# Kernel optimization log

Measured on AMD Instinct MI355X. Metric: run time of the kernel, lower is better.

## Reference

```python
import jax, jax.numpy as jnp
import numpy as np
from jax import lax

B, T, C = 4, 1024, 1024
NH, HD = 16, 64
SCALE = 1.0 / np.sqrt(HD)
LN_EPS = 1e-5


def _layernorm(x, g, b):
    mu = jnp.mean(x, axis=-1, keepdims=True)
    var = jnp.var(x, axis=-1, keepdims=True)
    return (x - mu) * lax.rsqrt(var + LN_EPS) * g + b


def _compress(seg, w, g, b):
    # seg: [B, nH, L, hd]; depthwise Conv1d(k=2, s=2, p=1, groups=hd, no bias) + LayerNorm(hd)
    Bs, nH, L, hd = seg.shape
    xc = seg.reshape(Bs * nH, L, hd).transpose(0, 2, 1)  # [B*nH, hd, L]
    y = lax.conv_general_dilated(xc, w, window_strides=(2,), padding=[(1, 1)],
                                 dimension_numbers=('NCH', 'OIH', 'NCH'),
                                 feature_group_count=hd)  # [B*nH, hd, L//2+1]
    y = y.transpose(0, 2, 1)
    y = _layernorm(y, g, b)
    return y.reshape(Bs, nH, -1, hd)


def setup_inputs() -> dict:
    key = jax.random.key(0)
    ks = jax.random.split(key, 16)
    d = {
        'x': jax.random.normal(ks[0], (B, T, C), jnp.float32),
        'mem_k1': jax.random.normal(ks[1], (B, NH, 129, HD), jnp.float32),
        'mem_v1': jax.random.normal(ks[2], (B, NH, 129, HD), jnp.float32),
        'mem_k2': jax.random.normal(ks[3], (B, NH, 257, HD), jnp.float32),
        'mem_v2': jax.random.normal(ks[4], (B, NH, 257, HD), jnp.float32),
        'mem_k3': jax.random.normal(ks[5], (B, NH, 513, HD), jnp.float32),
        'mem_v3': jax.random.normal(ks[6], (B, NH, 513, HD), jnp.float32),
        'c_attn_w': jax.random.normal(ks[7], (3 * C, C), jnp.float32) * 0.02,
        'c_attn_b': jnp.zeros((3 * C,), jnp.float32),
        'c_proj_w': jax.random.normal(ks[8], (C, C), jnp.float32) * 0.02,
        'c_proj_b': jnp.zeros((C,), jnp.float32),
        'compress_k_w': jax.random.normal(ks[9], (HD, 1, 2), jnp.float32) * 0.5,
        'ln_k_g': jnp.ones((HD,), jnp.float32),
        'ln_k_b': jnp.zeros((HD,), jnp.float32),
        'compress_v_w': jax.random.normal(ks[10], (HD, 1, 2), jnp.float32) * 0.5,
        'ln_v_g': jnp.ones((HD,), jnp.float32),
        'ln_v_b': jnp.zeros((HD,), jnp.float32),
    }
    return d


def reference(x, mem_k1, mem_v1, mem_k2, mem_v2, mem_k3, mem_v3,
              c_attn_w, c_attn_b, c_proj_w, c_proj_b,
              compress_k_w, ln_k_g, ln_k_b, compress_v_w, ln_v_g, ln_v_b):
    # qkv projection
    qkv = x @ c_attn_w.T + c_attn_b  # [B, T, 3C]
    q, k_new, v_new = jnp.split(qkv, 3, axis=2)
    q = q.reshape(B, T, NH, HD).transpose(0, 2, 1, 3)       # [B, nH, T, hd]
    k_new = k_new.reshape(B, T, NH, HD).transpose(0, 2, 1, 3)
    v_new = v_new.reshape(B, T, NH, HD).transpose(0, 2, 1, 3)

    # compress the most recent cached segment (513 -> 257)
    k3c = _compress(mem_k3, compress_k_w, ln_k_g, ln_k_b)
    v3c = _compress(mem_v3, compress_v_w, ln_v_g, ln_v_b)

    all_k = jnp.concatenate([mem_k1, mem_k2, k3c, k_new], axis=2)  # [B, nH, T_mem, hd]
    all_v = jnp.concatenate([mem_v1, mem_v2, v3c, v_new], axis=2)
    T_mem = all_k.shape[2]

    att = jnp.einsum('bhqd,bhkd->bhqk', q, all_k) * SCALE  # [B, nH, T, T_mem]
    # causal mask taken from tril(block_size)[:T, :T_mem]: row i attends cols j <= i
    mask = jnp.arange(T)[:, None] >= jnp.arange(T_mem)[None, :]
    att = jnp.where(mask, att, -jnp.inf)
    att = jax.nn.softmax(att, axis=-1)
    y = jnp.einsum('bhqk,bhkd->bhqd', att, all_v)  # [B, nH, T, hd]
    y = y.transpose(0, 2, 1, 3).reshape(B, T, C)
    y = y @ c_proj_w.T + c_proj_b
    return y
```

## Files before the change

kernel.cpp:

```cpp
#include <hip/hip_runtime.h>


using u16    = unsigned short;
using bf16x8 = __attribute__((ext_vector_type(8))) __bf16;
using f32x4  = __attribute__((ext_vector_type(4))) float;
using u16x8  = __attribute__((ext_vector_type(8))) unsigned short;
using u16x4  = __attribute__((ext_vector_type(4))) unsigned short;

__device__ __forceinline__ u16 f2bf(float f) {
    union { float f; unsigned u; } v; v.f = f;
    unsigned r = v.u + 0x7FFFu + ((v.u >> 16) & 1u);
    return (u16)(r >> 16);
}

__device__ __forceinline__ void gload16(const void* src, const void* lds_base) {
    __builtin_amdgcn_global_load_lds(
        (const __attribute__((address_space(1))) void*)src,
        (__attribute__((address_space(3))) void*)lds_base, 16, 0, 0);
}

__global__ void cvt_f32_bf16(const float* __restrict__ src, u16* __restrict__ dst, int n4) {
    int i = blockIdx.x * blockDim.x + threadIdx.x;
    if (i >= n4) return;
    float4 f = reinterpret_cast<const float4*>(src)[i];
    u16x4 o; o[0] = f2bf(f.x); o[1] = f2bf(f.y); o[2] = f2bf(f.z); o[3] = f2bf(f.w);
    reinterpret_cast<u16x4*>(dst)[i] = o;
}

__global__ __launch_bounds__(64) void copy_mem_rows(const float* __restrict__ src,
                                                    u16* __restrict__ dst, int L, int ro) {
    int bh = blockIdx.y, t = blockIdx.x, d = threadIdx.x;
    float v = src[((size_t)bh * L + t) * 64 + d];
    dst[((size_t)bh * 1024 + ro + t) * 64 + d] = f2bf(v);
}

__global__ __launch_bounds__(64) void compress_ln(const float* __restrict__ src,
                                                  const float* __restrict__ w,
                                                  const float* __restrict__ g,
                                                  const float* __restrict__ bta,
                                                  u16* __restrict__ dst, int ro) {
    int bh = blockIdx.y, t = blockIdx.x, d = threadIdx.x;
    const float* seg = src + (size_t)bh * 513 * 64;
    float x0 = (t > 0) ? seg[(size_t)(2 * t - 1) * 64 + d] : 0.f;
    float x1 = seg[(size_t)(2 * t) * 64 + d];
    float y = w[2 * d] * x0 + w[2 * d + 1] * x1;
    float s = y;
    #pragma unroll
    for (int o = 32; o; o >>= 1) s += __shfl_xor(s, o);
    float mu = s * (1.f / 64.f);
    float dv = y - mu;
    float s2 = dv * dv;
    #pragma unroll
    for (int o = 32; o; o >>= 1) s2 += __shfl_xor(s2, o);
    float var = s2 * (1.f / 64.f);
    float out = dv * rsqrtf(var + 1e-5f) * g[d] + bta[d];
    dst[((size_t)bh * 1024 + ro + t) * 64 + d] = f2bf(out);
}

__global__ __launch_bounds__(256) void transpose_v(const u16* __restrict__ src,
                                                   u16* __restrict__ dst) {
    __shared__ u16 tile[64][66];
    const int bh = blockIdx.y, t0 = blockIdx.x * 64;
    const int tid = threadIdx.x;
    #pragma unroll
    for (int i = 0; i < 2; ++i) {
        int p = tid + i * 256;
        int tr = p >> 3, dc = (p & 7) * 8;
        *(u16x8*)&tile[tr][dc] = *(const u16x8*)&src[((size_t)bh * 1024 + t0 + tr) * 64 + dc];
    }
    __syncthreads();
    #pragma unroll
    for (int i = 0; i < 2; ++i) {
        int p = tid + i * 256;
        int d = p >> 3, tc = (p & 7) * 8;
        u16x8 v;
        #pragma unroll
        for (int e = 0; e < 8; ++e) v[e] = tile[tc + e][d];
        *(u16x8*)&dst[((size_t)bh * 64 + d) * 1024 + t0 + tc] = v;
    }
}

__global__ __launch_bounds__(256) void gemm128(const u16* __restrict__ A,
                                               const u16* __restrict__ Bw,
                                               const float* __restrict__ bias,
                                               int K, int N, int mode,
                                               float* __restrict__ outF,
                                               u16* __restrict__ q_buf,
                                               u16* __restrict__ all_k,
                                               u16* __restrict__ all_v) {
    __shared__ __align__(16) u16 Al[3][128 * 32];
    __shared__ __align__(16) u16 Bl[3][128 * 32];
    const int tid = threadIdx.x;
    const int wv = tid >> 6, lane = tid & 63;
    const int lg = lane >> 4, lr = lane & 15;
    const int wr = (wv >> 1) * 64, wc = (wv & 1) * 64;
    const int id = blockIdx.x + blockIdx.y * gridDim.x;
    const int gx = gridDim.x;
    const int pm = gx >> 2;
    const int xcd = id & 7, lid = id >> 3;
    const int mg = xcd >> 1, ng = xcd & 1;
    const int lm = lid % pm, ln = lid / pm;
    const int m0 = (mg * pm + lm) * 128;
    const int n0 = (ng * (gridDim.y >> 1) + ln) * 128;
    f32x4 acc[4][4] = {};
    const int sr0 = tid >> 2,         sc0 = ((tid & 3) << 4) ^ (((sr0 >> 1) & 3) << 4);
    const int sr1 = (tid + 256) >> 2, sc1 = ((tid & 3) << 4) ^ (((sr1 >> 1) & 3) << 4);
    const int dA0 = wv * 1024;
    const int dA1 = 4096 + wv * 1024;
    const int nk = K >> 5;

    auto stage = [&](int j) {
        const size_t ko = (size_t)j << 5;
        char* Ad = (char*)&Al[j % 3][0];
        char* Bd = (char*)&Bl[j % 3][0];
        gload16((const char*)A  + (((size_t)(m0 + sr0) * K + ko) << 1) + sc0, Ad + dA0);
        gload16((const char*)A  + (((size_t)(m0 + sr1) * K + ko) << 1) + sc1, Ad + dA1);
        gload16((const char*)Bw + (((size_t)(n0 + sr0) * K + ko) << 1) + sc0, Bd + dA0);
        gload16((const char*)Bw + (((size_t)(n0 + sr1) * K + ko) << 1) + sc1, Bd + dA1);
    };
    stage(0);
    stage(1);
    asm volatile("s_waitcnt vmcnt(4)" ::: "memory");
    __builtin_amdgcn_s_barrier();
    __builtin_amdgcn_sched_barrier(0);

    for (int kt = 0; kt < nk; ++kt) {
        if (kt + 2 < nk) stage(kt + 2);
        const char* At = (const char*)&Al[kt % 3][0];
        const char* Bt = (const char*)&Bl[kt % 3][0];
        bf16x8 af[4], bq[4];
        #pragma unroll
        for (int mi = 0; mi < 4; ++mi) {
            int row = wr + mi * 16 + lr;
            af[mi] = *(const bf16x8*)(At + row * 64 + ((lg << 4) ^ (((row >> 1) & 3) << 4)));
        }
        #pragma unroll
        for (int ni = 0; ni < 4; ++ni) {
            int row = wc + ni * 16 + lr;
            bq[ni] = *(const bf16x8*)(Bt + row * 64 + ((lg << 4) ^ (((row >> 1) & 3) << 4)));
        }
        __builtin_amdgcn_s_setprio(1);
        #pragma unroll
        for (int mi = 0; mi < 4; ++mi)
            #pragma unroll
            for (int ni = 0; ni < 4; ++ni)
                acc[mi][ni] = __builtin_amdgcn_mfma_f32_16x16x32_bf16(af[mi], bq[ni], acc[mi][ni], 0, 0, 0);
        __builtin_amdgcn_s_setprio(0);
        if (kt + 1 < nk) {
            if (kt + 2 < nk) {
                asm volatile("s_waitcnt vmcnt(4)" ::: "memory");
            } else {
                asm volatile("s_waitcnt vmcnt(0)" ::: "memory");
            }
            __builtin_amdgcn_s_barrier();
            __builtin_amdgcn_sched_barrier(0);
        }
    }
    #pragma unroll
    for (int mi = 0; mi < 4; ++mi)
        #pragma unroll
        for (int ni = 0; ni < 4; ++ni)
            #pragma unroll
            for (int r = 0; r < 4; ++r) {
                int mm = m0 + wr + mi * 16 + lg * 4 + r;
                int nn = n0 + wc + ni * 16 + lr;
                float v = acc[mi][ni][r] + bias[nn];
                if (mode == 0) {
                    outF[(size_t)mm * N + nn] = v;
                } else {
                    int which = nn >> 10, c = nn & 1023, h = c >> 6, d = c & 63;
                    int b = mm >> 10, t = mm & 1023;
                    int bh = b * 16 + h;
                    if (which == 0) {
                        q_buf[((size_t)bh * 1024 + t) * 64 + d] = f2bf(v * 0.125f);
                    } else if (t < 381) {
                        u16* dst = (which == 1) ? all_k : all_v;
                        dst[((size_t)bh * 1024 + 643 + t) * 64 + d] = f2bf(v);
                    }
                }
            }
}

__global__ __launch_bounds__(256) void attn_kernel(const u16* __restrict__ Q,
                                                   const u16* __restrict__ Kc,
                                                   const u16* __restrict__ VT,
                                                   u16* __restrict__ Y) {
    __shared__ __align__(16) u16 Kl[2][4096];
    __shared__ __align__(16) u16 Vl[2][4096];
    __shared__ __align__(16) u16 P_w[4][16 * 64];
    const int tid = threadIdx.x;
    const int lane = tid & 63;
    const int w = tid >> 6;
    const int lg = lane >> 4, lr = lane & 15;
    const int bh = blockIdx.x;
    const int pair = blockIdx.y;
    const u16* Kb = Kc + (size_t)bh * 65536;
    const u16* Vb = VT + (size_t)bh * 65536;
    char* Pbase = (char*)&P_w[w][0];
    const int xorq = (lr & 7) << 4;

    const int r0 = tid >> 3,         c0 = ((tid & 7) * 16) ^ ((r0 & 7) << 4);
    const int r1 = (tid + 256) >> 3, c1 = ((tid & 7) * 16) ^ ((r1 & 7) << 4);
    const int dst0 = w * 1024;

    for (int phase = 0; phase < 2; ++phase) {
        const int qt = phase ? (15 - pair) : pair;
        const int q0 = qt * 64;
        const u16* Qb = Q + ((size_t)bh * 1024 + q0 + w * 16) * 64;
        bf16x8 qf0 = *(const bf16x8*)&Qb[lr * 64 + lg * 8];
        bf16x8 qf1 = *(const bf16x8*)&Qb[lr * 64 + 32 + lg * 8];
        f32x4 o[4] = {};
        float m = -1e30f, lsum = 0.f;
        const int i_q = q0 + w * 16 + lr;

        {
            const char* Ks = (const char*)Kb;
            gload16(Ks + ((size_t)r0 << 7) + c0, (char*)&Kl[0][0] + dst0);
            gload16(Ks + ((size_t)r1 << 7) + c1, (char*)&Kl[0][0] + 4096 + dst0);
            gload16((const char*)Vb + ((size_t)r0 << 11) + c0, (char*)&Vl[0][0] + dst0);
            gload16((const char*)Vb + ((size_t)r1 << 11) + c1, (char*)&Vl[0][0] + 4096 + dst0);
        }
        __syncthreads();
        int cur = 0;

        for (int kt = 0; kt <= qt; ++kt) {
            if (kt < qt) {
                const int k0n = (kt + 1) * 64;
                const char* Ks = (const char*)Kb + ((size_t)k0n << 7);
                const char* Vs = (const char*)Vb + ((size_t)k0n << 1);
                char* Kd = (char*)&Kl[cur ^ 1][0];
                char* Vd = (char*)&Vl[cur ^ 1][0];
                gload16(Ks + ((size_t)r0 << 7) + c0, Kd + dst0);
                gload16(Ks + ((size_t)r1 << 7) + c1, Kd + 4096 + dst0);
                gload16(Vs + ((size_t)r0 << 11) + c0, Vd + dst0);
                gload16(Vs + ((size_t)r1 << 11) + c1, Vd + 4096 + dst0);
            }
            const char* Kt = (const char*)&Kl[cur][0];
            const char* Vt = (const char*)&Vl[cur][0];
            f32x4 st[4] = {};
            __builtin_amdgcn_s_setprio(1);
            #pragma unroll
            for (int hh = 0; hh < 4; ++hh) {
                const char* Kr = Kt + (size_t)(hh * 16 + lr) * 128;
                bf16x8 kf0 = *(const bf16x8*)(Kr + ((lg * 16) ^ xorq));
                bf16x8 kf1 = *(const bf16x8*)(Kr + ((64 + lg * 16) ^ xorq));
                st[hh] = __builtin_amdgcn_mfma_f32_16x16x32_bf16(kf0, qf0, st[hh], 0, 0, 0);
                st[hh] = __builtin_amdgcn_mfma_f32_16x16x32_bf16(kf1, qf1, st[hh], 0, 0, 0);
            }
            __builtin_amdgcn_s_setprio(0);
            const int k0 = kt * 64;
            float sv[16];
            float tmax = -1e30f;
            if (kt == qt) {
                #pragma unroll
                for (int hh = 0; hh < 4; ++hh)
                    #pragma unroll
                    for (int r = 0; r < 4; ++r) {
                        int j = k0 + hh * 16 + lg * 4 + r;
                        float s = (j <= i_q) ? st[hh][r] : -1e30f;
                        sv[hh * 4 + r] = s;
                        tmax = fmaxf(tmax, s);
                    }
            } else {
                #pragma unroll
                for (int hh = 0; hh < 4; ++hh)
                    #pragma unroll
                    for (int r = 0; r < 4; ++r) {
                        float s = st[hh][r];
                        sv[hh * 4 + r] = s;
                        tmax = fmaxf(tmax, s);
                    }
            }
            tmax = fmaxf(tmax, __shfl_xor(tmax, 16));
            tmax = fmaxf(tmax, __shfl_xor(tmax, 32));
            if (!__all(tmax - m <= 8.f)) {
                float mnew = fmaxf(m, tmax);
                float alpha = __expf(m - mnew);
                #pragma unroll
                for (int c = 0; c < 4; ++c) {
                    o[c][0] *= alpha; o[c][1] *= alpha; o[c][2] *= alpha; o[c][3] *= alpha;
                }
                lsum *= alpha;
                m = mnew;
            }
            float psum = 0.f;
            #pragma unroll
            for (int hh = 0; hh < 4; ++hh) {
                u16x4 pk;
                #pragma unroll
                for (int r = 0; r < 4; ++r) {
                    float p = __expf(sv[hh * 4 + r] - m);
                    psum += p;
                    pk[r] = f2bf(p);
                }
                *(u16x4*)(Pbase + lr * 128 + ((hh * 32 + lg * 8) ^ xorq)) = pk;
            }
            psum += __shfl_xor(psum, 16);
            psum += __shfl_xor(psum, 32);
            lsum += psum;
            asm volatile("s_waitcnt lgkmcnt(0)" ::: "memory");
            __builtin_amdgcn_sched_barrier(0);
            #pragma unroll
            for (int ks = 0; ks < 2; ++ks) {
                bf16x8 pf = *(const bf16x8*)(Pbase + lr * 128 + ((ks * 64 + lg * 16) ^ xorq));
                __builtin_amdgcn_s_setprio(1);
                #pragma unroll
                for (int c = 0; c < 4; ++c) {
                    const char* Vr = Vt + (size_t)(c * 16 + lr) * 128;
                    bf16x8 vf = *(const bf16x8*)(Vr + ((ks * 64 + lg * 16) ^ xorq));
                    o[c] = __builtin_amdgcn_mfma_f32_16x16x32_bf16(vf, pf, o[c], 0, 0, 0);
                }
                __builtin_amdgcn_s_setprio(0);
            }
            __syncthreads();
            cur ^= 1;
        }
        float inv = 1.0f / lsum;
        #pragma unroll
        for (int c = 0; c < 4; ++c) {
            u16x4 ov;
            #pragma unroll
            for (int r = 0; r < 4; ++r) ov[r] = f2bf(o[c][r] * inv);
            *(u16x4*)(Pbase + lr * 128 + (((c * 16 + lg * 4) * 2) ^ xorq)) = ov;
        }
        asm volatile("s_waitcnt lgkmcnt(0)" ::: "memory");
        __builtin_amdgcn_sched_barrier(0);
        const int b = bh >> 4, h = bh & 15;
        const int qr = lane >> 2, dseg = (lane & 3) * 16;
        const int xorr = (qr & 7) << 4;
        size_t g = ((size_t)(b * 1024 + q0 + w * 16 + qr)) * 1024 + h * 64 + dseg;
        *(u16x8*)&Y[g]     = *(const u16x8*)(Pbase + qr * 128 + ((dseg * 2) ^ xorr));
        *(u16x8*)&Y[g + 8] = *(const u16x8*)(Pbase + qr * 128 + ((dseg * 2 + 16) ^ xorr));
    }
}

extern "C" void kernel_launch(void* const* d_in, const int* in_sizes, int n_in,
                              void* d_out, int out_size, void* d_ws, size_t ws_size,
                              hipStream_t stream) {
    const float* x            = (const float*)d_in[0];
    const float* mem_k1       = (const float*)d_in[1];
    const float* mem_v1       = (const float*)d_in[2];
    const float* mem_k2       = (const float*)d_in[3];
    const float* mem_v2       = (const float*)d_in[4];
    const float* mem_k3       = (const float*)d_in[5];
    const float* mem_v3       = (const float*)d_in[6];
    const float* c_attn_w     = (const float*)d_in[7];
    const float* c_attn_b     = (const float*)d_in[8];
    const float* c_proj_w     = (const float*)d_in[9];
    const float* c_proj_b     = (const float*)d_in[10];
    const float* compress_k_w = (const float*)d_in[11];
    const float* ln_k_g       = (const float*)d_in[12];
    const float* ln_k_b       = (const float*)d_in[13];
    const float* compress_v_w = (const float*)d_in[14];
    const float* ln_v_g       = (const float*)d_in[15];
    const float* ln_v_b       = (const float*)d_in[16];

    char* ws = (char*)d_ws;
    u16* x_bf   = (u16*)(ws);
    u16* all_vT = (u16*)(ws);
    u16* wq_bf  = (u16*)(ws + (8u << 20));
    u16* wp_bf  = (u16*)(ws + (14u << 20));
    u16* q_buf  = (u16*)(ws + (16u << 20));
    u16* all_k  = (u16*)(ws + (24u << 20));
    u16* all_v  = (u16*)(ws + (32u << 20));
    u16* att_y  = (u16*)(ws + (40u << 20));
    float* out = (float*)d_out;

    cvt_f32_bf16<<<4096, 256, 0, stream>>>(x, x_bf, 1048576);
    cvt_f32_bf16<<<3072, 256, 0, stream>>>(c_attn_w, wq_bf, 786432);
    cvt_f32_bf16<<<1024, 256, 0, stream>>>(c_proj_w, wp_bf, 262144);

    copy_mem_rows<<<dim3(129, 64), 64, 0, stream>>>(mem_k1, all_k, 129, 0);
    copy_mem_rows<<<dim3(129, 64), 64, 0, stream>>>(mem_v1, all_v, 129, 0);
    copy_mem_rows<<<dim3(257, 64), 64, 0, stream>>>(mem_k2, all_k, 257, 129);
    copy_mem_rows<<<dim3(257, 64), 64, 0, stream>>>(mem_v2, all_v, 257, 129);

    compress_ln<<<dim3(257, 64), 64, 0, stream>>>(mem_k3, compress_k_w, ln_k_g, ln_k_b, all_k, 386);
    compress_ln<<<dim3(257, 64), 64, 0, stream>>>(mem_v3, compress_v_w, ln_v_g, ln_v_b, all_v, 386);

    gemm128<<<dim3(32, 24), 256, 0, stream>>>(x_bf, wq_bf, c_attn_b, 1024, 3072, 1,
                                              nullptr, q_buf, all_k, all_v);

    transpose_v<<<dim3(16, 64), 256, 0, stream>>>(all_v, all_vT);

    attn_kernel<<<dim3(64, 8), 256, 0, stream>>>(q_buf, all_k, all_vT, att_y);

    gemm128<<<dim3(32, 8), 256, 0, stream>>>(att_y, wp_bf, c_proj_b, 1024, 1024, 0,
                                             out, nullptr, nullptr, nullptr);
}
```

Measured before the change: 139.6 us.

## Enlarge GEMM tiles to 128x256 with BK=64 and 8 waves per block

Replaces the 128x128, BK=32 GEMM with a 128x256 output tile and a K-step of 64, using 512 threads (8 waves), a single 48KB-per-stage triple-buffered LDS ring, and a new row-xor swizzle for 128-byte rows. Block-to-XCD remapping is simplified to a contiguous chunk per XCD. The aim is more reuse per loaded tile and fewer barriers per K. The cost is 144KB of LDS per block and fewer blocks (384 and 128), which may leave CUs idle on the smaller projection GEMM.

```diff
diff --git a/kernel.cpp b/kernel.cpp
--- a/kernel.cpp
+++ b/kernel.cpp
@@ -80,7 +80,7 @@
     }
 }
 
-__global__ __launch_bounds__(256) void gemm128(const u16* __restrict__ A,
+__global__ __launch_bounds__(512) void gemm256(const u16* __restrict__ A,
                                                const u16* __restrict__ Bw,
                                                const float* __restrict__ bias,
                                                int K, int N, int mode,
@@ -88,67 +88,74 @@
                                                u16* __restrict__ q_buf,
                                                u16* __restrict__ all_k,
                                                u16* __restrict__ all_v) {
-    __shared__ __align__(16) u16 Al[3][128 * 32];
-    __shared__ __align__(16) u16 Bl[3][128 * 32];
+    __shared__ __align__(16) char ring[3][49152];
     const int tid = threadIdx.x;
     const int wv = tid >> 6, lane = tid & 63;
     const int lg = lane >> 4, lr = lane & 15;
-    const int wr = (wv >> 1) * 64, wc = (wv & 1) * 64;
+    const int wr = (wv >> 2) * 64, wc = (wv & 3) * 64;
     const int id = blockIdx.x + blockIdx.y * gridDim.x;
     const int gx = gridDim.x;
-    const int pm = gx >> 2;
-    const int xcd = id & 7, lid = id >> 3;
-    const int mg = xcd >> 1, ng = xcd & 1;
-    const int lm = lid % pm, ln = lid / pm;
-    const int m0 = (mg * pm + lm) * 128;
-    const int n0 = (ng * (gridDim.y >> 1) + ln) * 128;
+    const int per = (gx * gridDim.y) >> 3;
+    const int nid = (id & 7) * per + (id >> 3);
+    const int m0 = (nid % gx) * 128;
+    const int n0 = (nid / gx) * 256;
     f32x4 acc[4][4] = {};
-    const int sr0 = tid >> 2,         sc0 = ((tid & 3) << 4) ^ (((sr0 >> 1) & 3) << 4);
-    const int sr1 = (tid + 256) >> 2, sc1 = ((tid & 3) << 4) ^ (((sr1 >> 1) & 3) << 4);
-    const int dA0 = wv * 1024;
-    const int dA1 = 4096 + wv * 1024;
-    const int nk = K >> 5;
-
+    int srow[6], scol[6], sdst[6];
+    #pragma unroll
+    for (int c = 0; c < 6; ++c) {
+        int chunk = (c < 2) ? (c * 8 + wv) : ((c - 2) * 8 + wv);
+        int s = chunk * 64 + lane;
+        int row = s >> 3;
+        srow[c] = row;
+        scol[c] = ((s & 7) << 4) ^ ((row & 7) << 4);
+        sdst[c] = (c < 2) ? (chunk * 1024) : (16384 + chunk * 1024);
+    }
+    const int nk = K >> 6;
     auto stage = [&](int j) {
-        const size_t ko = (size_t)j << 5;
-        char* Ad = (char*)&Al[j % 3][0];
-        char* Bd = (char*)&Bl[j % 3][0];
-        gload16((const char*)A  + (((size_t)(m0 + sr0) * K + ko) << 1) + sc0, Ad + dA0);
-        gload16((const char*)A  + (((size_t)(m0 + sr1) * K + ko) << 1) + sc1, Ad + dA1);
-        gload16((const char*)Bw + (((size_t)(n0 + sr0) * K + ko) << 1) + sc0, Bd + dA0);
-        gload16((const char*)Bw + (((size_t)(n0 + sr1) * K + ko) << 1) + sc1, Bd + dA1);
+        char* base = ring[j % 3];
+        const size_t ko = (size_t)j << 6;
+        #pragma unroll
+        for (int c = 0; c < 6; ++c) {
+            const u16* src = (c < 2) ? A : Bw;
+            const int rb = (c < 2) ? m0 : n0;
+            gload16((const char*)src + (((size_t)(rb + srow[c]) * K + ko) << 1) + scol[c],
+                    base + sdst[c]);
+        }
     };
     stage(0);
     stage(1);
-    asm volatile("s_waitcnt vmcnt(4)" ::: "memory");
+    asm volatile("s_waitcnt vmcnt(6)" ::: "memory");
     __builtin_amdgcn_s_barrier();
     __builtin_amdgcn_sched_barrier(0);
 
     for (int kt = 0; kt < nk; ++kt) {
         if (kt + 2 < nk) stage(kt + 2);
-        const char* At = (const char*)&Al[kt % 3][0];
-        const char* Bt = (const char*)&Bl[kt % 3][0];
-        bf16x8 af[4], bq[4];
-        #pragma unroll
-        for (int mi = 0; mi < 4; ++mi) {
-            int row = wr + mi * 16 + lr;
-            af[mi] = *(const bf16x8*)(At + row * 64 + ((lg << 4) ^ (((row >> 1) & 3) << 4)));
-        }
-        #pragma unroll
-        for (int ni = 0; ni < 4; ++ni) {
-            int row = wc + ni * 16 + lr;
-            bq[ni] = *(const bf16x8*)(Bt + row * 64 + ((lg << 4) ^ (((row >> 1) & 3) << 4)));
-        }
-        __builtin_amdgcn_s_setprio(1);
-        #pragma unroll
-        for (int mi = 0; mi < 4; ++mi)
-            #pragma unroll
-            for (int ni = 0; ni < 4; ++ni)
-                acc[mi][ni] = __builtin_amdgcn_mfma_f32_16x16x32_bf16(af[mi], bq[ni], acc[mi][ni], 0, 0, 0);
-        __builtin_amdgcn_s_setprio(0);
+        const char* At = ring[kt % 3];
+        const char* Bt = ring[kt % 3] + 16384;
+        #pragma unroll
+        for (int dh = 0; dh < 2; ++dh) {
+            bf16x8 af[4], bq[4];
+            #pragma unroll
+            for (int mi = 0; mi < 4; ++mi) {
+                int row = wr + mi * 16 + lr;
+                af[mi] = *(const bf16x8*)(At + row * 128 + ((dh * 64 + lg * 16) ^ ((row & 7) << 4)));
+            }
+            #pragma unroll
+            for (int ni = 0; ni < 4; ++ni) {
+                int row = wc + ni * 16 + lr;
+                bq[ni] = *(const bf16x8*)(Bt + row * 128 + ((dh * 64 + lg * 16) ^ ((row & 7) << 4)));
+            }
+            __builtin_amdgcn_s_setprio(1);
+            #pragma unroll
+            for (int mi = 0; mi < 4; ++mi)
+                #pragma unroll
+                for (int ni = 0; ni < 4; ++ni)
+                    acc[mi][ni] = __builtin_amdgcn_mfma_f32_16x16x32_bf16(af[mi], bq[ni], acc[mi][ni], 0, 0, 0);
+            __builtin_amdgcn_s_setprio(0);
+        }
         if (kt + 1 < nk) {
             if (kt + 2 < nk) {
-                asm volatile("s_waitcnt vmcnt(4)" ::: "memory");
+                asm volatile("s_waitcnt vmcnt(6)" ::: "memory");
             } else {
                 asm volatile("s_waitcnt vmcnt(0)" ::: "memory");
             }
@@ -378,13 +385,13 @@
     compress_ln<<<dim3(257, 64), 64, 0, stream>>>(mem_k3, compress_k_w, ln_k_g, ln_k_b, all_k, 386);
     compress_ln<<<dim3(257, 64), 64, 0, stream>>>(mem_v3, compress_v_w, ln_v_g, ln_v_b, all_v, 386);
 
-    gemm128<<<dim3(32, 24), 256, 0, stream>>>(x_bf, wq_bf, c_attn_b, 1024, 3072, 1,
+    gemm256<<<dim3(32, 12), 512, 0, stream>>>(x_bf, wq_bf, c_attn_b, 1024, 3072, 1,
                                               nullptr, q_buf, all_k, all_v);
 
     transpose_v<<<dim3(16, 64), 256, 0, stream>>>(all_v, all_vT);
 
     attn_kernel<<<dim3(64, 8), 256, 0, stream>>>(q_buf, all_k, all_vT, att_y);
 
-    gemm128<<<dim3(32, 8), 256, 0, stream>>>(att_y, wp_bf, c_proj_b, 1024, 1024, 0,
+    gemm256<<<dim3(32, 4), 512, 0, stream>>>(att_y, wp_bf, c_proj_b, 1024, 1024, 0,
                                              out, nullptr, nullptr, nullptr);
 }
```

New measurement: 144.9 us. +3.8%, slower.
